# Optimization experiments

Hardware: AMD Instinct MI355X
Metric: run time of the kernel (lower is better)

The kernel has to match this reference:

```python
import jax, jax.numpy as jnp
import numpy as np


def floor_ste(x):
    # forward: floor(x); backward: identity (straight-through estimator)
    return x + jax.lax.stop_gradient(jnp.floor(x) - x)


def _int_polynomial(x_int, sf):
    c0, c1, c2 = 0.35815147, 0.96963238, 1.0
    b_int = floor_ste((c1 / c0) / sf)
    c_int = floor_ste((c2 / c0) / (sf * sf))
    z = x_int * (x_int + b_int) + c_int
    return z, c0 * sf * sf


def _int_exp(x_int, sf):
    x0 = -0.69314718
    n = 15
    x0_int = floor_ste(x0 / sf)
    x_int = jnp.maximum(x_int, n * x0_int)
    q = floor_ste(x_int / x0_int)
    r = x_int - x0_int * q
    exp_int, exp_sf = _int_polynomial(r, sf)
    exp_int = jnp.maximum(floor_ste(exp_int * jnp.exp2(n - q)), 0.0)
    return exp_int, exp_sf / (2.0 ** n)


def _int_softmax(x, sf):
    x_int = x / sf
    x_int = x_int - jnp.max(x_int, axis=-1, keepdims=True)
    exp_int, exp_sf = _int_exp(x_int, sf)
    exp_int_sum = jnp.sum(exp_int, axis=-1, keepdims=True)
    return exp_int, exp_int_sum, exp_sf


def setup_inputs() -> dict:
    key = jax.random.key(0)
    k1, = jax.random.split(key, 1)
    x = jax.random.normal(k1, (2, 16, 1024, 1024), dtype=jnp.float32)
    scale = jnp.float32(0.05)          # activation quantization step
    threshold = jnp.array([0.1], dtype=jnp.float32)  # nn.Parameter init
    return {"x": x, "scale": scale, "threshold": threshold}


def reference(x, scale, threshold):
    output_bit = 8
    threshold_bits = 8
    exp_int, exp_int_sum, exp_sf = _int_softmax(x, scale)
    factor = floor_ste((2.0 ** 32) / exp_int_sum)
    out_scale_A = threshold / (2.0 ** output_bit - 1.0)   # shape [1]
    out_scale_B = 1.0 / (2.0 ** output_bit - 1.0)
    approx_threshold = (floor_ste(threshold * 2.0 ** threshold_bits)
                        * exp_int_sum / (2.0 ** threshold_bits))
    mask_A = exp_int <= approx_threshold
    exp_int_A = jnp.where(mask_A, exp_int, 0.0)
    exp_int_B = jnp.where(mask_A, 0.0, exp_int)
    softmax_int_A = floor_ste(exp_int_A * factor / ((2.0 ** 32) * out_scale_A))
    softmax_int_B = floor_ste(exp_int_B * factor / ((2.0 ** 32) * out_scale_B))
    softmax_int_B = jnp.minimum(softmax_int_B, 255.0)
    return softmax_int_A * out_scale_A + softmax_int_B * out_scale_B
```

## Files before the change

kernel.cpp:

```cpp
#include <hip/hip_runtime.h>
#include <math.h>

#pragma clang fp contract(off)

#define TPB 256
#define ROWLEN 1024
#define PERSIST_BLOCKS 2048

typedef float f32x4 __attribute__((ext_vector_type(4)));

__device__ __forceinline__ float wave_max_dpp(float m) {
    const int NEG_INF = 0xff800000;
    int v;
    v = __builtin_amdgcn_update_dpp(NEG_INF, __float_as_int(m), 0x111, 0xf, 0xf, false);
    m = fmaxf(m, __int_as_float(v));
    v = __builtin_amdgcn_update_dpp(NEG_INF, __float_as_int(m), 0x112, 0xf, 0xf, false);
    m = fmaxf(m, __int_as_float(v));
    v = __builtin_amdgcn_update_dpp(NEG_INF, __float_as_int(m), 0x114, 0xf, 0xf, false);
    m = fmaxf(m, __int_as_float(v));
    v = __builtin_amdgcn_update_dpp(NEG_INF, __float_as_int(m), 0x118, 0xf, 0xf, false);
    m = fmaxf(m, __int_as_float(v));
    v = __builtin_amdgcn_update_dpp(NEG_INF, __float_as_int(m), 0x142, 0xa, 0xf, false);
    m = fmaxf(m, __int_as_float(v));
    v = __builtin_amdgcn_update_dpp(NEG_INF, __float_as_int(m), 0x143, 0xc, 0xf, false);
    m = fmaxf(m, __int_as_float(v));
    return __int_as_float(__builtin_amdgcn_readlane(__float_as_int(m), 63));
}

__device__ __forceinline__ unsigned wave_sum_dpp_u32(unsigned a) {
    int v;
    v = __builtin_amdgcn_update_dpp(0, (int)a, 0x111, 0xf, 0xf, false); a += (unsigned)v;
    v = __builtin_amdgcn_update_dpp(0, (int)a, 0x112, 0xf, 0xf, false); a += (unsigned)v;
    v = __builtin_amdgcn_update_dpp(0, (int)a, 0x114, 0xf, 0xf, false); a += (unsigned)v;
    v = __builtin_amdgcn_update_dpp(0, (int)a, 0x118, 0xf, 0xf, false); a += (unsigned)v;
    v = __builtin_amdgcn_update_dpp(0, (int)a, 0x142, 0xa, 0xf, false); a += (unsigned)v;
    v = __builtin_amdgcn_update_dpp(0, (int)a, 0x143, 0xc, 0xf, false); a += (unsigned)v;
    return (unsigned)__builtin_amdgcn_readlane((int)a, 63);
}

__global__ __launch_bounds__(TPB) void qsplit_int_softmax_kernel(
    const float* __restrict__ x,
    const float* __restrict__ scale_p,
    const float* __restrict__ thr_p,
    float* __restrict__ out,
    const int rows)
{
    const int tid  = threadIdx.x;
    const int lane = tid & 63;
    const int wid  = tid >> 6;

    __shared__ float  smax[4];
    __shared__ double ssum[4];

    const float sf  = scale_p[0];
    const float thr = thr_p[0];

    const float rh = 1.0f / sf;
    const float er = __builtin_fmaf(-sf, rh, 1.0f);
    const float rl = rh * er;

    #define DF_DIV(a) ({ float _p = (a) * rh; \
                         float _e = __builtin_fmaf((a), rh, -_p); \
                         _p + __builtin_fmaf((a), rl, _e); })
    const float x0f    = floorf(DF_DIV(-0.69314718f));
    const float bfc    = floorf(DF_DIV(2.7073824f));
    const float s2     = sf * sf;
    const float r2h    = 1.0f / s2;
    const float r2e    = __builtin_fmaf(-s2, r2h, 1.0f);
    const float r2l    = r2h * r2e;
    const float cq     = __builtin_fmaf(2.7921141f, r2l,
                         2.7921141f * r2h);
    const float cfc    = floorf(cq);
    const float clampf = 15.0f * x0f;
    const float invx0f = 1.0f / x0f;

    const float osA  = thr / 255.0f;
    const float osB  = 1.0f / 255.0f;
    const float invA = 1.0f / (4294967296.0f * osA);
    const float invB = 1.0f / (4294967296.0f * osB);
    const float thrq = floorf(thr * 256.0f);

    const int stride = gridDim.x;
    int r = blockIdx.x;
    if (r >= rows) return;

    f32x4 xv = *(const f32x4*)(x + (size_t)r * ROWLEN + (size_t)tid * 4);

    for (;;) {
        const int rn = r + stride;
        const bool has_next = (rn < rows);
        f32x4 xn;
        if (has_next)
            xn = *(const f32x4*)(x + (size_t)rn * ROWLEN + (size_t)tid * 4);

        float xi[4];
        #pragma unroll
        for (int j = 0; j < 4; ++j) {
            const float xx = xv[j];
            const float p  = xx * rh;
            const float e  = __builtin_fmaf(xx, rh, -p);
            xi[j] = p + __builtin_fmaf(xx, rl, e);
        }

        float m = fmaxf(fmaxf(xi[0], xi[1]), fmaxf(xi[2], xi[3]));
        m = wave_max_dpp(m);
        if (lane == 0) smax[wid] = m;
        __syncthreads();
        m = fmaxf(fmaxf(smax[0], smax[1]), fmaxf(smax[2], smax[3]));

        float e4[4];
        unsigned usum = 0;
        #pragma unroll
        for (int j = 0; j < 4; ++j) {
            float v = xi[j] - m;
            v = fmaxf(v, clampf);
            const float qf = floorf(v * invx0f);
            const int   qi = (int)qf;
            const float rr = v - x0f * qf;
            const float t  = rr + bfc;
            const float z  = rr * t + cfc;
            float ei = floorf(ldexpf(z, 15 - qi));
            ei = fmaxf(ei, 0.0f);
            e4[j] = ei;
            usum += (unsigned)ei;
        }

        const unsigned lo = wave_sum_dpp_u32(usum & 0xFFFFu);
        const unsigned hi = wave_sum_dpp_u32(usum >> 16);
        if (lane == 0)
            ssum[wid] = (double)(((unsigned long long)hi << 16) + lo);
        __syncthreads();
        const double s = ((ssum[0] + ssum[1]) + ssum[2]) + ssum[3];

        const float fac_f = (float)floor(4294967296.0 / s);
        const float ath_f = (float)(((double)thrq * s) * (1.0 / 256.0));

        f32x4 o;
        #pragma unroll
        for (int j = 0; j < 4; ++j) {
            const float ei  = e4[j];
            const bool  isA = (ei <= ath_f);
            const float t1  = ei * fac_f;
            const float t2  = t1 * (isA ? invA : invB);
            float si = floorf(t2);
            si = fminf(si, isA ? 3.0e38f : 255.0f);
            o[j] = si * (isA ? osA : osB);
        }
        __builtin_nontemporal_store(o, (f32x4*)(out + (size_t)r * ROWLEN + (size_t)tid * 4));

        if (!has_next) break;
        r  = rn;
        xv = xn;
    }
}

extern "C" void kernel_launch(void* const* d_in, const int* in_sizes, int n_in,
                              void* d_out, int out_size, void* d_ws, size_t ws_size,
                              hipStream_t stream) {
    const float* x     = (const float*)d_in[0];
    const float* scale = (const float*)d_in[1];
    const float* thr   = (const float*)d_in[2];
    float* out = (float*)d_out;

    const int total = in_sizes[0];
    const int rows  = total / ROWLEN;

    const int blocks = rows < PERSIST_BLOCKS ? rows : PERSIST_BLOCKS;

    qsplit_int_softmax_kernel<<<dim3(blocks), dim3(TPB), 0, stream>>>(
        x, scale, thr, out, rows);
}
```

Measured before the change: 235.2 us.

## Map one row per wavefront to remove block-level barriers and shared memory

Each 64-lane wavefront now handles a whole 1024-element row with 16 values per lane, so the max and sum reductions finish entirely within the wave using DPP and no longer need shared memory or __syncthreads. The persistent grid strides by wavefronts, the next row is prefetched into registers, and uniform constants are broadcast with readfirstlane so they can live in scalar registers. Launch bounds now request 8 blocks per CU. Register use roughly quadruples (cur plus nxt), which could limit occupancy, and each wave has more serial work per row.

```diff
diff --git a/kernel.cpp b/kernel.cpp
--- a/kernel.cpp
+++ b/kernel.cpp
@@ -8,6 +8,10 @@
 #define PERSIST_BLOCKS 2048
 
 typedef float f32x4 __attribute__((ext_vector_type(4)));
+
+static __device__ __forceinline__ float bcast_f32(float v) {
+    return __int_as_float(__builtin_amdgcn_readfirstlane(__float_as_int(v)));
+}
 
 __device__ __forceinline__ float wave_max_dpp(float m) {
     const int NEG_INF = 0xff800000;
@@ -38,7 +42,7 @@
     return (unsigned)__builtin_amdgcn_readlane((int)a, 63);
 }
 
-__global__ __launch_bounds__(TPB) void qsplit_int_softmax_kernel(
+__global__ __launch_bounds__(TPB, 8) void qsplit_int_softmax_kernel(
     const float* __restrict__ x,
     const float* __restrict__ scale_p,
     const float* __restrict__ thr_p,
@@ -48,71 +52,85 @@
     const int tid  = threadIdx.x;
     const int lane = tid & 63;
     const int wid  = tid >> 6;
-
-    __shared__ float  smax[4];
-    __shared__ double ssum[4];
+    const int nw   = (int)(gridDim.x << 2);
+    int r = (int)(blockIdx.x << 2) | wid;
 
     const float sf  = scale_p[0];
     const float thr = thr_p[0];
 
-    const float rh = 1.0f / sf;
+    const float rh = bcast_f32(1.0f / sf);
     const float er = __builtin_fmaf(-sf, rh, 1.0f);
-    const float rl = rh * er;
+    const float rl = bcast_f32(rh * er);
 
     #define DF_DIV(a) ({ float _p = (a) * rh; \
                          float _e = __builtin_fmaf((a), rh, -_p); \
                          _p + __builtin_fmaf((a), rl, _e); })
-    const float x0f    = floorf(DF_DIV(-0.69314718f));
-    const float bfc    = floorf(DF_DIV(2.7073824f));
+    const float x0f    = bcast_f32(floorf(DF_DIV(-0.69314718f)));
+    const float bfc    = bcast_f32(floorf(DF_DIV(2.7073824f)));
     const float s2     = sf * sf;
     const float r2h    = 1.0f / s2;
     const float r2e    = __builtin_fmaf(-s2, r2h, 1.0f);
     const float r2l    = r2h * r2e;
     const float cq     = __builtin_fmaf(2.7921141f, r2l,
                          2.7921141f * r2h);
-    const float cfc    = floorf(cq);
-    const float clampf = 15.0f * x0f;
-    const float invx0f = 1.0f / x0f;
+    const float cfc    = bcast_f32(floorf(cq));
+    const float clampf = bcast_f32(15.0f * x0f);
+    const float invx0f = bcast_f32(1.0f / x0f);
 
-    const float osA  = thr / 255.0f;
-    const float osB  = 1.0f / 255.0f;
-    const float invA = 1.0f / (4294967296.0f * osA);
-    const float invB = 1.0f / (4294967296.0f * osB);
-    const float thrq = floorf(thr * 256.0f);
+    const float osA  = bcast_f32(thr / 255.0f);
+    const float osB  = bcast_f32(1.0f / 255.0f);
+    const float invA = bcast_f32(1.0f / (4294967296.0f * osA));
+    const float invB = bcast_f32(1.0f / (4294967296.0f * osB));
+    const float thrq = bcast_f32(floorf(thr * 256.0f));
 
-    const int stride = gridDim.x;
-    int r = blockIdx.x;
     if (r >= rows) return;
 
-    f32x4 xv = *(const f32x4*)(x + (size_t)r * ROWLEN + (size_t)tid * 4);
+    const size_t step = (size_t)nw * ROWLEN;
+    const float* px = x   + (size_t)r * ROWLEN + ((size_t)lane << 2);
+    float*       po = out + (size_t)r * ROWLEN + ((size_t)lane << 2);
+
+    float cur[16];
+    #pragma unroll
+    for (int g = 0; g < 4; ++g) {
+        const f32x4 v = *(const f32x4*)(px + (g << 8));
+        cur[4*g+0] = v[0]; cur[4*g+1] = v[1];
+        cur[4*g+2] = v[2]; cur[4*g+3] = v[3];
+    }
 
     for (;;) {
-        const int rn = r + stride;
-        const bool has_next = (rn < rows);
-        f32x4 xn;
-        if (has_next)
-            xn = *(const f32x4*)(x + (size_t)rn * ROWLEN + (size_t)tid * 4);
+        const bool has_next = (r + nw < rows);
+        float nxt[16];
+        if (has_next) {
+            const float* pn = px + step;
+            #pragma unroll
+            for (int g = 0; g < 4; ++g) {
+                const f32x4 v = *(const f32x4*)(pn + (g << 8));
+                nxt[4*g+0] = v[0]; nxt[4*g+1] = v[1];
+                nxt[4*g+2] = v[2]; nxt[4*g+3] = v[3];
+            }
+        }
 
-        float xi[4];
         #pragma unroll
-        for (int j = 0; j < 4; ++j) {
-            const float xx = xv[j];
+        for (int j = 0; j < 16; ++j) {
+            const float xx = cur[j];
             const float p  = xx * rh;
             const float e  = __builtin_fmaf(xx, rh, -p);
-            xi[j] = p + __builtin_fmaf(xx, rl, e);
+            cur[j] = p + __builtin_fmaf(xx, rl, e);
         }
 
-        float m = fmaxf(fmaxf(xi[0], xi[1]), fmaxf(xi[2], xi[3]));
-        m = wave_max_dpp(m);
-        if (lane == 0) smax[wid] = m;
-        __syncthreads();
-        m = fmaxf(fmaxf(smax[0], smax[1]), fmaxf(smax[2], smax[3]));
+        float t0 = fmaxf(cur[0], cur[1]),  t1 = fmaxf(cur[2], cur[3]);
+        float t2 = fmaxf(cur[4], cur[5]),  t3 = fmaxf(cur[6], cur[7]);
+        float t4 = fmaxf(cur[8], cur[9]),  t5 = fmaxf(cur[10], cur[11]);
+        float t6 = fmaxf(cur[12], cur[13]),t7 = fmaxf(cur[14], cur[15]);
+        t0 = fmaxf(t0, t1); t2 = fmaxf(t2, t3);
+        t4 = fmaxf(t4, t5); t6 = fmaxf(t6, t7);
+        t0 = fmaxf(t0, t2); t4 = fmaxf(t4, t6);
+        const float m = wave_max_dpp(fmaxf(t0, t4));
 
-        float e4[4];
         unsigned usum = 0;
         #pragma unroll
-        for (int j = 0; j < 4; ++j) {
-            float v = xi[j] - m;
+        for (int j = 0; j < 16; ++j) {
+            float v = cur[j] - m;
             v = fmaxf(v, clampf);
             const float qf = floorf(v * invx0f);
             const int   qi = (int)qf;
@@ -121,36 +139,38 @@
             const float z  = rr * t + cfc;
             float ei = floorf(ldexpf(z, 15 - qi));
             ei = fmaxf(ei, 0.0f);
-            e4[j] = ei;
+            cur[j] = ei;
             usum += (unsigned)ei;
         }
 
         const unsigned lo = wave_sum_dpp_u32(usum & 0xFFFFu);
         const unsigned hi = wave_sum_dpp_u32(usum >> 16);
-        if (lane == 0)
-            ssum[wid] = (double)(((unsigned long long)hi << 16) + lo);
-        __syncthreads();
-        const double s = ((ssum[0] + ssum[1]) + ssum[2]) + ssum[3];
+        const double s = (double)(((unsigned long long)hi << 16) + lo);
 
-        const float fac_f = (float)floor(4294967296.0 / s);
-        const float ath_f = (float)(((double)thrq * s) * (1.0 / 256.0));
+        const float fac_f = bcast_f32((float)floor(4294967296.0 / s));
+        const float ath_f = bcast_f32((float)(((double)thrq * s) * (1.0 / 256.0)));
 
-        f32x4 o;
         #pragma unroll
-        for (int j = 0; j < 4; ++j) {
-            const float ei  = e4[j];
-            const bool  isA = (ei <= ath_f);
-            const float t1  = ei * fac_f;
-            const float t2  = t1 * (isA ? invA : invB);
-            float si = floorf(t2);
-            si = fminf(si, isA ? 3.0e38f : 255.0f);
-            o[j] = si * (isA ? osA : osB);
+        for (int g = 0; g < 4; ++g) {
+            f32x4 o;
+            #pragma unroll
+            for (int jj = 0; jj < 4; ++jj) {
+                const float ei  = cur[4*g+jj];
+                const bool  isA = (ei <= ath_f);
+                const float t1_ = ei * fac_f;
+                const float t2_ = t1_ * (isA ? invA : invB);
+                float si = floorf(t2_);
+                si = fminf(si, isA ? 3.0e38f : 255.0f);
+                o[jj] = si * (isA ? osA : osB);
+            }
+            __builtin_nontemporal_store(o, (f32x4*)(po + (g << 8)));
         }
-        __builtin_nontemporal_store(o, (f32x4*)(out + (size_t)r * ROWLEN + (size_t)tid * 4));
 
         if (!has_next) break;
-        r  = rn;
-        xv = xn;
+        r  += nw;
+        px += step; po += step;
+        #pragma unroll
+        for (int j = 0; j < 16; ++j) cur[j] = nxt[j];
     }
 }
 
@@ -165,7 +185,8 @@
     const int total = in_sizes[0];
     const int rows  = total / ROWLEN;
 
-    const int blocks = rows < PERSIST_BLOCKS ? rows : PERSIST_BLOCKS;
+    const int wave_blocks = (rows + 3) / 4;
+    const int blocks = wave_blocks < PERSIST_BLOCKS ? wave_blocks : PERSIST_BLOCKS;
 
     qsplit_int_softmax_kernel<<<dim3(blocks), dim3(TPB), 0, stream>>>(
         x, scale, thr, out, rows);
```

Measured after the change: 236.2 us. About the same (+0.4%).
